# Optimization experiments

Hardware: AMD Instinct MI355X
Metric: run time of the kernel (lower is better)

## Reference

```python
import jax, jax.numpy as jnp
import numpy as np
from jax import lax

B, T = 256, 512
D_DEC, D_ENC2, D_ATT = 512, 1024, 128
N_FILT, K = 32, 31
PAD = (K - 1) // 2


def setup_inputs() -> dict:
    key = jax.random.key(0)
    ks = jax.random.split(key, 10)
    s = 0.02
    return {
        "query": jax.random.normal(ks[0], (B, D_DEC), jnp.float32),
        "encoder_output": jax.random.normal(ks[1], (B, T, D_ENC2), jnp.float32),
        "attention_weights": jax.random.uniform(ks[2], (B, T), jnp.float32),
        "Wq": jax.random.normal(ks[3], (D_DEC, D_ATT), jnp.float32) * s,
        "Wk": jax.random.normal(ks[4], (D_ENC2, D_ATT), jnp.float32) * s,
        "Wv": jax.random.normal(ks[5], (D_ENC2, D_DEC), jnp.float32) * s,
        "Wloc": jax.random.normal(ks[6], (N_FILT, D_ATT), jnp.float32) * s,
        "conv_w": jax.random.normal(ks[7], (N_FILT, 1, K), jnp.float32) * s,
        "conv_b": jax.random.normal(ks[8], (N_FILT,), jnp.float32) * s,
        "Wscore": jax.random.normal(ks[9], (D_ATT, 1), jnp.float32) * s,
    }


def reference(query, encoder_output, attention_weights, Wq, Wk, Wv, Wloc, conv_w, conv_b, Wscore):
    # query projection: (B, D_att), broadcast over time
    q = (query @ Wq)[:, None, :]                      # (B, 1, D_att)
    k = encoder_output @ Wk                           # (B, T, D_att)
    # location features: conv1d over previous attention weights
    loc = lax.conv_general_dilated(
        attention_weights[:, None, :],                # (B, 1, T)
        conv_w,                                       # (F, 1, K)
        window_strides=(1,),
        padding=[(PAD, PAD)],
        dimension_numbers=("NCH", "OIH", "NCH"),
    ) + conv_b[None, :, None]                         # (B, F, T)
    loc = jnp.einsum("bft,fa->bta", loc, Wloc)        # (B, T, D_att)
    energy = jnp.tanh(q + k + loc) @ Wscore           # (B, T, 1)
    new_w = jax.nn.softmax(energy[..., 0], axis=1)    # (B, T)
    context = jnp.einsum("bt,btd->bd", new_w, encoder_output) @ Wv  # (B, D_dec)
    return context, new_w
```

## Files before the change

kernel.cpp:

```cpp
#include <hip/hip_runtime.h>
#include <hip/hip_bf16.h>

typedef __attribute__((ext_vector_type(8))) short bf16x8;
typedef __attribute__((ext_vector_type(4))) float f32x4;

#define NB   256
#define TT   512
#define DDEC 512
#define DENC 1024
#define DATT 128
#define NF   32
#define KW   31
#define PW   15

struct SMem {
  union {
    struct {
      __hip_bfloat16 locA[512][40];
      __hip_bfloat16 locBt[128][40];
    } l;
    float part[16][1024];
  } u;
  float qpart[8][128];
  float attw[TT];
  float qrow[DDEC];
  float cw[NF][32];
  float cb[NF];
  float qv[DATT];
  float wsc[DATT];
  float energy[TT];
  float red[16];
  float scal[2];
};

__device__ __forceinline__ float fast_tanh(float x) {
  float e = __expf(2.f * x);
  return 1.f - 2.f / (e + 1.f);
}

__global__ __launch_bounds__(256) void prep_wkt(const float* __restrict__ Wk,
                                                __hip_bfloat16* __restrict__ WkT) {
  int idx = blockIdx.x * 256 + threadIdx.x;
  int k2 = idx >> 7, a = idx & 127;
  int k = k2 * 2;
  union { ushort2 u; __hip_bfloat16 h[2]; } cv;
  cv.h[0] = __float2bfloat16(Wk[(size_t)k * DATT + a]);
  cv.h[1] = __float2bfloat16(Wk[(size_t)(k + 1) * DATT + a]);
  *reinterpret_cast<ushort2*>(WkT + (size_t)a * 1024 + k) = cv.u;
}

__global__ __launch_bounds__(1024) void pass1_kernel(
    const float* __restrict__ query,
    const float* __restrict__ enc,
    const float* __restrict__ attw,
    const float* __restrict__ Wq,
    const __hip_bfloat16* __restrict__ WkT,
    const float* __restrict__ Wloc,
    const float* __restrict__ convw,
    const float* __restrict__ convb,
    const float* __restrict__ wscore,
    float* __restrict__ out_w,
    float* __restrict__ ctx_enc) {
  __shared__ SMem sm;
  const int b    = blockIdx.x;
  const int tid  = threadIdx.x;
  const int lane = tid & 63;
  const int wv   = tid >> 6;
  const int lrow = lane & 15;
  const int lgrp = lane >> 4;

  if (tid < TT) {
    sm.attw[tid] = attw[(size_t)b * TT + tid];
    sm.qrow[tid] = query[(size_t)b * DDEC + tid];
  }
  if (tid < NF * KW) sm.cw[tid / KW][tid % KW] = convw[tid];
  if (tid < NF)   sm.cb[tid]  = convb[tid];
  if (tid < DATT) sm.wsc[tid] = wscore[tid];
  for (int i = tid; i < NF * DATT; i += 1024) {
    int f = i >> 7, a = i & 127;
    sm.u.l.locBt[a][f] = __float2bfloat16(Wloc[i]);
  }
  __syncthreads();

  {
    const int p = tid >> 7, a = tid & 127;
    float acc = 0.f;
    const float* wq = Wq + (size_t)(p * 64) * DATT + a;
#pragma unroll 8
    for (int d = 0; d < 64; ++d)
      acc = fmaf(sm.qrow[p * 64 + d], wq[(size_t)d * DATT], acc);
    sm.qpart[p][a] = acc;
  }
  {
    const int t = tid & 511, h = tid >> 9;
#pragma unroll
    for (int f0 = 0; f0 < 16; ++f0) {
      const int f = h * 16 + f0;
      float acc = sm.cb[f];
      for (int k = 0; k < KW; ++k) {
        int ts = t - PW + k;
        float x = (ts >= 0 && ts < TT) ? sm.attw[ts] : 0.f;
        acc = fmaf(sm.cw[f][k], x, acc);
      }
      sm.u.l.locA[t][f] = __float2bfloat16(acc);
    }
  }
  __syncthreads();
  if (tid < DATT) {
    float s = 0.f;
#pragma unroll
    for (int p = 0; p < 8; ++p) s += sm.qpart[p][tid];
    sm.qv[tid] = s;
  }

  f32x4 acc[2][8];
  {
    bf16x8 af[2], bfr[8];
#pragma unroll
    for (int m = 0; m < 2; ++m)
      af[m] = *reinterpret_cast<const bf16x8*>(
          &sm.u.l.locA[wv * 32 + m * 16 + lrow][lgrp * 8]);
#pragma unroll
    for (int n = 0; n < 8; ++n)
      bfr[n] = *reinterpret_cast<const bf16x8*>(
          &sm.u.l.locBt[n * 16 + lrow][lgrp * 8]);
#pragma unroll
    for (int m = 0; m < 2; ++m)
#pragma unroll
      for (int n = 0; n < 8; ++n)
        acc[m][n] = __builtin_amdgcn_mfma_f32_16x16x32_bf16(
            af[m], bfr[n], (f32x4){0.f, 0.f, 0.f, 0.f}, 0, 0, 0);
  }
  __syncthreads();

  const float* pa0 = enc + (((size_t)b * TT) + wv * 32 + lrow) * DENC + lgrp * 8;
  const __hip_bfloat16* pb = WkT + lrow * 1024 + lgrp * 8;

  for (int c = 0; c < 16; ++c) {
    const int k0 = c * 64;
#pragma unroll
    for (int s = 0; s < 2; ++s) {
      const int ko = k0 + s * 32;
      bf16x8 af[2];
#pragma unroll
      for (int m = 0; m < 2; ++m) {
        const float* p = pa0 + (size_t)m * 16 * DENC + ko;
        float4 v0 = *reinterpret_cast<const float4*>(p);
        float4 v1 = *reinterpret_cast<const float4*>(p + 4);
        union { bf16x8 v; __hip_bfloat16 h[8]; } cv;
        cv.h[0] = __float2bfloat16(v0.x); cv.h[1] = __float2bfloat16(v0.y);
        cv.h[2] = __float2bfloat16(v0.z); cv.h[3] = __float2bfloat16(v0.w);
        cv.h[4] = __float2bfloat16(v1.x); cv.h[5] = __float2bfloat16(v1.y);
        cv.h[6] = __float2bfloat16(v1.z); cv.h[7] = __float2bfloat16(v1.w);
        af[m] = cv.v;
      }
      bf16x8 bfr[8];
#pragma unroll
      for (int n = 0; n < 8; ++n)
        bfr[n] = *reinterpret_cast<const bf16x8*>(pb + (size_t)n * 16 * 1024 + ko);
#pragma unroll
      for (int m = 0; m < 2; ++m)
#pragma unroll
        for (int n = 0; n < 8; ++n)
          acc[m][n] = __builtin_amdgcn_mfma_f32_16x16x32_bf16(
              af[m], bfr[n], acc[m][n], 0, 0, 0);
    }
  }

#pragma unroll
  for (int m = 0; m < 2; ++m) {
#pragma unroll
    for (int r = 0; r < 4; ++r) {
      float e = 0.f;
#pragma unroll
      for (int n = 0; n < 8; ++n) {
        int col = n * 16 + lrow;
        float v = acc[m][n][r] + sm.qv[col];
        e = fmaf(fast_tanh(v), sm.wsc[col], e);
      }
      e += __shfl_xor(e, 1);
      e += __shfl_xor(e, 2);
      e += __shfl_xor(e, 4);
      e += __shfl_xor(e, 8);
      if (lrow == 0) sm.energy[wv * 32 + m * 16 + lgrp * 4 + r] = e;
    }
  }
  __syncthreads();

  const float e0 = (tid < TT) ? sm.energy[tid] : -1e30f;
  float m1 = e0;
#pragma unroll
  for (int off = 1; off < 64; off <<= 1) m1 = fmaxf(m1, __shfl_xor(m1, off));
  if (lane == 0) sm.red[wv] = m1;
  __syncthreads();
  if (tid == 0) {
    float mm = sm.red[0];
#pragma unroll
    for (int i = 1; i < 16; ++i) mm = fmaxf(mm, sm.red[i]);
    sm.scal[0] = mm;
  }
  __syncthreads();
  const float ex = (tid < TT) ? __expf(e0 - sm.scal[0]) : 0.f;
  float s1 = ex;
#pragma unroll
  for (int off = 1; off < 64; off <<= 1) s1 += __shfl_xor(s1, off);
  if (lane == 0) sm.red[wv] = s1;
  __syncthreads();
  if (tid == 0) {
    float ss = 0.f;
#pragma unroll
    for (int i = 0; i < 16; ++i) ss += sm.red[i];
    sm.scal[1] = 1.f / ss;
  }
  __syncthreads();
  if (tid < TT) {
    const float wnorm = ex * sm.scal[1];
    sm.energy[tid] = wnorm;
    out_w[(size_t)b * TT + tid] = wnorm;
  }
  __syncthreads();

  float4 a0 = {0,0,0,0}, a1 = {0,0,0,0}, a2 = {0,0,0,0}, a3 = {0,0,0,0};
  const int t0 = wv * 32;
  for (int tt = 0; tt < 32; ++tt) {
    const int t = t0 + tt;
    const float wt = sm.energy[t];
    const float4* row =
        reinterpret_cast<const float4*>(enc + ((size_t)b * TT + t) * DENC);
    float4 v0 = row[lane];
    float4 v1 = row[64 + lane];
    float4 v2 = row[128 + lane];
    float4 v3 = row[192 + lane];
    a0.x = fmaf(wt, v0.x, a0.x); a0.y = fmaf(wt, v0.y, a0.y);
    a0.z = fmaf(wt, v0.z, a0.z); a0.w = fmaf(wt, v0.w, a0.w);
    a1.x = fmaf(wt, v1.x, a1.x); a1.y = fmaf(wt, v1.y, a1.y);
    a1.z = fmaf(wt, v1.z, a1.z); a1.w = fmaf(wt, v1.w, a1.w);
    a2.x = fmaf(wt, v2.x, a2.x); a2.y = fmaf(wt, v2.y, a2.y);
    a2.z = fmaf(wt, v2.z, a2.z); a2.w = fmaf(wt, v2.w, a2.w);
    a3.x = fmaf(wt, v3.x, a3.x); a3.y = fmaf(wt, v3.y, a3.y);
    a3.z = fmaf(wt, v3.z, a3.z); a3.w = fmaf(wt, v3.w, a3.w);
  }
  *reinterpret_cast<float4*>(&sm.u.part[wv][lane * 4])       = a0;
  *reinterpret_cast<float4*>(&sm.u.part[wv][256 + lane * 4]) = a1;
  *reinterpret_cast<float4*>(&sm.u.part[wv][512 + lane * 4]) = a2;
  *reinterpret_cast<float4*>(&sm.u.part[wv][768 + lane * 4]) = a3;
  __syncthreads();
  {
    const int d = tid;
    float s = 0.f;
#pragma unroll
    for (int w = 0; w < 16; ++w) s += sm.u.part[w][d];
    ctx_enc[(size_t)b * DENC + d] = s;
  }
}

__global__ __launch_bounds__(512) void ctx_proj_kernel(
    const float* __restrict__ ctx_enc,
    const float* __restrict__ Wv,
    float* __restrict__ out) {
  __shared__ float sc[DENC];
  const int b = blockIdx.x, tid = threadIdx.x;
  for (int i = tid; i < DENC; i += 512) sc[i] = ctx_enc[(size_t)b * DENC + i];
  __syncthreads();
  float acc = 0.f;
#pragma unroll 8
  for (int d = 0; d < DENC; ++d)
    acc = fmaf(sc[d], Wv[(size_t)d * DDEC + tid], acc);
  out[(size_t)b * DDEC + tid] = acc;
}

extern "C" void kernel_launch(void* const* d_in, const int* in_sizes, int n_in,
                              void* d_out, int out_size, void* d_ws, size_t ws_size,
                              hipStream_t stream) {
  const float* query  = (const float*)d_in[0];
  const float* enc    = (const float*)d_in[1];
  const float* attw   = (const float*)d_in[2];
  const float* Wq     = (const float*)d_in[3];
  const float* Wk     = (const float*)d_in[4];
  const float* Wv     = (const float*)d_in[5];
  const float* Wloc   = (const float*)d_in[6];
  const float* convw  = (const float*)d_in[7];
  const float* convb  = (const float*)d_in[8];
  const float* wscore = (const float*)d_in[9];

  float* ctx     = (float*)d_out;
  float* neww    = (float*)d_out + NB * TT;
  float* ctx_enc = (float*)d_ws;
  __hip_bfloat16* WkT =
      (__hip_bfloat16*)((char*)d_ws + (size_t)NB * DENC * sizeof(float));

  hipLaunchKernelGGL(prep_wkt, dim3(256), dim3(256), 0, stream, Wk, WkT);
  hipLaunchKernelGGL(pass1_kernel, dim3(NB), dim3(1024), 0, stream,
                     query, enc, attw, Wq, WkT, Wloc, convw, convb, wscore,
                     neww, ctx_enc);
  hipLaunchKernelGGL(ctx_proj_kernel, dim3(NB), dim3(512), 0, stream,
                     ctx_enc, Wv, ctx);
}
```

Baseline: 390.9 us.

## Double-buffer encoder tiles into LDS via async global_load_lds in K-loop

Replaces the direct per-lane float4 global loads of encoder rows in the key-projection MFMA loop with asynchronous global-to-LDS copies, using a per-wave double buffer and an XOR swizzle. The next 32-column chunk is prefetched while the current one is converted to bf16 and fed to the MFMAs, with explicit vmcnt waits and scheduling barriers. The aim is to hide global memory latency on the dominant encoder stream. It adds 128KB of LDS use through the union and relies on hand-counted vmcnt values, which could lower occupancy or break if the load counts change.

After: 353.7 us. 1.11x faster.

```diff
diff --git a/kernel.cpp b/kernel.cpp
--- a/kernel.cpp
+++ b/kernel.cpp
@@ -13,12 +13,18 @@
 #define KW   31
 #define PW   15
 
+#define GLDS16(g, l)                                                        \
+  __builtin_amdgcn_global_load_lds(                                         \
+      (const __attribute__((address_space(1))) void*)(uintptr_t)(g),        \
+      (__attribute__((address_space(3))) void*)(uintptr_t)(l), 16, 0, 0)
+
 struct SMem {
   union {
     struct {
       __hip_bfloat16 locA[512][40];
       __hip_bfloat16 locBt[128][40];
     } l;
+    char astage[16 * 8192];
     float part[16][1024];
   } u;
   float qpart[8][128];
@@ -133,39 +139,70 @@
   }
   __syncthreads();
 
-  const float* pa0 = enc + (((size_t)b * TT) + wv * 32 + lrow) * DENC + lgrp * 8;
-  const __hip_bfloat16* pb = WkT + lrow * 1024 + lgrp * 8;
-
-  for (int c = 0; c < 16; ++c) {
-    const int k0 = c * 64;
-#pragma unroll
-    for (int s = 0; s < 2; ++s) {
-      const int ko = k0 + s * 32;
-      bf16x8 af[2];
-#pragma unroll
-      for (int m = 0; m < 2; ++m) {
-        const float* p = pa0 + (size_t)m * 16 * DENC + ko;
-        float4 v0 = *reinterpret_cast<const float4*>(p);
-        float4 v1 = *reinterpret_cast<const float4*>(p + 4);
-        union { bf16x8 v; __hip_bfloat16 h[8]; } cv;
-        cv.h[0] = __float2bfloat16(v0.x); cv.h[1] = __float2bfloat16(v0.y);
-        cv.h[2] = __float2bfloat16(v0.z); cv.h[3] = __float2bfloat16(v0.w);
-        cv.h[4] = __float2bfloat16(v1.x); cv.h[5] = __float2bfloat16(v1.y);
-        cv.h[6] = __float2bfloat16(v1.z); cv.h[7] = __float2bfloat16(v1.w);
-        af[m] = cv.v;
-      }
-      bf16x8 bfr[8];
+  char* abase = sm.u.astage + wv * 8192;
+  const int srow  = lane >> 3;
+  const int swcol = ((lane & 7) ^ srow) * 4;
+  const float* gs = enc + ((size_t)b * TT + wv * 32 + srow) * DENC + swcol;
+
+  auto STAGE = [&](int p, int c) {
+    const float* g0 = gs + c * 32;
+    char* d0 = abase + p * 4096;
+#pragma unroll
+    for (int i = 0; i < 4; ++i)
+      GLDS16(g0 + (size_t)i * 8 * DENC, d0 + i * 1024);
+  };
+
+  bf16x8 bfr[8];
+  auto LOADB = [&](int c) {
+    const __hip_bfloat16* pbc = WkT + (size_t)lrow * 1024 + lgrp * 8 + c * 32;
+#pragma unroll
+    for (int n = 0; n < 8; ++n)
+      bfr[n] = *reinterpret_cast<const bf16x8*>(pbc + (size_t)n * 16 * 1024);
+  };
+
+  auto COMPUTE = [&](int cur) {
+    const char* rb = abase + cur * 4096;
+    bf16x8 af[2];
+#pragma unroll
+    for (int m = 0; m < 2; ++m) {
+      const int row = m * 16 + lrow;
+      const int x = (row & 7) << 4;
+      float4 f0 = *reinterpret_cast<const float4*>(
+          rb + row * 128 + ((lgrp * 32) ^ x));
+      float4 f1 = *reinterpret_cast<const float4*>(
+          rb + row * 128 + ((lgrp * 32 + 16) ^ x));
+      union { bf16x8 v; __hip_bfloat16 h[8]; } cv;
+      cv.h[0] = __float2bfloat16(f0.x); cv.h[1] = __float2bfloat16(f0.y);
+      cv.h[2] = __float2bfloat16(f0.z); cv.h[3] = __float2bfloat16(f0.w);
+      cv.h[4] = __float2bfloat16(f1.x); cv.h[5] = __float2bfloat16(f1.y);
+      cv.h[6] = __float2bfloat16(f1.z); cv.h[7] = __float2bfloat16(f1.w);
+      af[m] = cv.v;
+    }
+#pragma unroll
+    for (int m = 0; m < 2; ++m)
 #pragma unroll
       for (int n = 0; n < 8; ++n)
-        bfr[n] = *reinterpret_cast<const bf16x8*>(pb + (size_t)n * 16 * 1024 + ko);
-#pragma unroll
-      for (int m = 0; m < 2; ++m)
-#pragma unroll
-        for (int n = 0; n < 8; ++n)
-          acc[m][n] = __builtin_amdgcn_mfma_f32_16x16x32_bf16(
-              af[m], bfr[n], acc[m][n], 0, 0, 0);
-    }
-  }
+        acc[m][n] = __builtin_amdgcn_mfma_f32_16x16x32_bf16(
+            af[m], bfr[n], acc[m][n], 0, 0, 0);
+  };
+
+  STAGE(0, 0);
+  int cur = 0;
+#pragma unroll 1
+  for (int c = 0; c < 31; ++c) {
+    LOADB(c);
+    STAGE(cur ^ 1, c + 1);
+    __builtin_amdgcn_sched_barrier(0);
+    asm volatile("s_waitcnt vmcnt(12)" ::: "memory");
+    __builtin_amdgcn_sched_barrier(0);
+    COMPUTE(cur);
+    cur ^= 1;
+  }
+  LOADB(31);
+  __builtin_amdgcn_sched_barrier(0);
+  asm volatile("s_waitcnt vmcnt(8)" ::: "memory");
+  __builtin_amdgcn_sched_barrier(0);
+  COMPUTE(cur);
 
 #pragma unroll
   for (int m = 0; m < 2; ++m) {
```

## Rewrite main kernel as single-pass flash-style online softmax with LDS-staged encoder tiles

Applied to the files above, without the earlier changes.

Replaces the two-read structure (energy GEMM reading encoder rows, then a second global pass for the weighted context sum) with a tiled loop over time. Each 16-row tile is double-buffered into LDS via global_load_lds with an XOR swizzle, then reused for both the Wk projection (MFMA, split-K across waves with LDS atomic adds) and the context accumulation, using an online max/sum softmax. This is meant to halve global reads of the large encoder tensor and overlap loads with compute. In exchange it adds per-tile barriers, LDS atomics, a split-K reduction, and rescaling work, and the location features are recomputed per tile with scalar loops.

Result: slower. 1.285 ms (+228.7%).

```diff
diff --git a/kernel.cpp b/kernel.cpp
--- a/kernel.cpp
+++ b/kernel.cpp
@@ -12,30 +12,46 @@
 #define NF   32
 #define KW   31
 #define PW   15
+#define TR   16
+#define NTILE 32
+
+#define GLDS16(g, l)                                                        \
+  __builtin_amdgcn_global_load_lds(                                         \
+      (const __attribute__((address_space(1))) void*)(uintptr_t)(g),        \
+      (__attribute__((address_space(3))) void*)(uintptr_t)(l), 16, 0, 0)
 
 struct SMem {
-  union {
-    struct {
-      __hip_bfloat16 locA[512][40];
-      __hip_bfloat16 locBt[128][40];
-    } l;
-    float part[16][1024];
-  } u;
-  float qpart[8][128];
+  float buf[2][TR][1024];
+  float E[TR][137];
+  __hip_bfloat16 wlocT[DATT][36];
   float attw[TT];
   float qrow[DDEC];
-  float cw[NF][32];
+  float cw[NF][KW + 1];
   float cb[NF];
   float qv[DATT];
   float wsc[DATT];
-  float energy[TT];
-  float red[16];
-  float scal[2];
+  float locf[TR][34];
+  float e_red[TR];
+  float e_save[TT];
 };
 
 __device__ __forceinline__ float fast_tanh(float x) {
   float e = __expf(2.f * x);
   return 1.f - 2.f / (e + 1.f);
+}
+
+__device__ __forceinline__ void memfence_sched() {
+  __builtin_amdgcn_sched_barrier(0);
+  asm volatile("" ::: "memory");
+}
+__device__ __forceinline__ void bar_raw() {
+  memfence_sched();
+  __builtin_amdgcn_s_barrier();
+  memfence_sched();
+}
+__device__ __forceinline__ void bar_lgkm() {
+  asm volatile("s_waitcnt lgkmcnt(0)" ::: "memory");
+  bar_raw();
 }
 
 __global__ __launch_bounds__(256) void prep_wkt(const float* __restrict__ Wk,
@@ -49,10 +65,10 @@
   *reinterpret_cast<ushort2*>(WkT + (size_t)a * 1024 + k) = cv.u;
 }
 
-__global__ __launch_bounds__(1024) void pass1_kernel(
+__global__ __launch_bounds__(1024) void flash_kernel(
     const float* __restrict__ query,
     const float* __restrict__ enc,
-    const float* __restrict__ attw,
+    const float* __restrict__ attwg,
     const float* __restrict__ Wq,
     const __hip_bfloat16* __restrict__ WkT,
     const float* __restrict__ Wloc,
@@ -62,15 +78,13 @@
     float* __restrict__ out_w,
     float* __restrict__ ctx_enc) {
   __shared__ SMem sm;
-  const int b    = blockIdx.x;
-  const int tid  = threadIdx.x;
-  const int lane = tid & 63;
-  const int wv   = tid >> 6;
-  const int lrow = lane & 15;
-  const int lgrp = lane >> 4;
+  const int b = blockIdx.x, tid = threadIdx.x;
+  const int lane = tid & 63, wv = tid >> 6;
+  const int lrow = lane & 15, lgrp = lane >> 4;
+  const int ks = wv >> 1, ch = wv & 1;
 
   if (tid < TT) {
-    sm.attw[tid] = attw[(size_t)b * TT + tid];
+    sm.attw[tid] = attwg[(size_t)b * TT + tid];
     sm.qrow[tid] = query[(size_t)b * DDEC + tid];
   }
   if (tid < NF * KW) sm.cw[tid / KW][tid % KW] = convw[tid];
@@ -78,180 +92,162 @@
   if (tid < DATT) sm.wsc[tid] = wscore[tid];
   for (int i = tid; i < NF * DATT; i += 1024) {
     int f = i >> 7, a = i & 127;
-    sm.u.l.locBt[a][f] = __float2bfloat16(Wloc[i]);
-  }
-  __syncthreads();
+    sm.wlocT[a][f] = __float2bfloat16(Wloc[i]);
+  }
+
+  bf16x8 bfr[4][4];
+#pragma unroll
+  for (int s = 0; s < 4; ++s)
+#pragma unroll
+    for (int n = 0; n < 4; ++n)
+      bfr[s][n] = *reinterpret_cast<const bf16x8*>(
+          WkT + (size_t)(ch * 64 + n * 16 + lrow) * 1024 + ks * 128 + s * 32 + lgrp * 8);
+
+  auto STAGE = [&](int p, int t) {
+    const float* gsrc = enc + ((size_t)b * TT + t * TR + wv) * DENC;
+    char* dst = (char*)&sm.buf[p][wv][0];
+    const int swz = ((lane & 7) ^ (wv & 7)) | (lane & 56);
+#pragma unroll
+    for (int i = 0; i < 4; ++i)
+      GLDS16(gsrc + (size_t)(i * 64 + swz) * 4, dst + i * 1024);
+  };
+
+  STAGE(0, 0);
+  bar_lgkm();
 
   {
+    float* qp = &sm.E[0][0];
     const int p = tid >> 7, a = tid & 127;
     float acc = 0.f;
     const float* wq = Wq + (size_t)(p * 64) * DATT + a;
 #pragma unroll 8
-    for (int d = 0; d < 64; ++d)
-      acc = fmaf(sm.qrow[p * 64 + d], wq[(size_t)d * DATT], acc);
-    sm.qpart[p][a] = acc;
-  }
+    for (int dd = 0; dd < 64; ++dd)
+      acc = fmaf(sm.qrow[p * 64 + dd], wq[(size_t)dd * DATT], acc);
+    qp[p * 128 + a] = acc;
+  }
+  bar_lgkm();
+  if (tid < DATT) {
+    float* qp = &sm.E[0][0];
+    float s = 0.f;
+#pragma unroll
+    for (int p = 0; p < 8; ++p) s += qp[p * 128 + tid];
+    sm.qv[tid] = s;
+  }
+  bar_lgkm();
   {
-    const int t = tid & 511, h = tid >> 9;
-#pragma unroll
-    for (int f0 = 0; f0 < 16; ++f0) {
-      const int f = h * 16 + f0;
-      float acc = sm.cb[f];
-      for (int k = 0; k < KW; ++k) {
-        int ts = t - PW + k;
-        float x = (ts >= 0 && ts < TT) ? sm.attw[ts] : 0.f;
-        acc = fmaf(sm.cw[f][k], x, acc);
+    int i0 = tid * 2;
+    sm.E[i0 >> 7][i0 & 127] = 0.f;
+    sm.E[(i0 + 1) >> 7][(i0 + 1) & 127] = 0.f;
+  }
+  bar_lgkm();
+
+  float m_run = -INFINITY, l_run = 0.f, ctxv = 0.f;
+  const int d = tid;
+
+#pragma unroll 1
+  for (int t = 0; t < NTILE; ++t) {
+    const int cur = t & 1;
+    if (t + 1 < NTILE) {
+      STAGE(cur ^ 1, t + 1);
+      __builtin_amdgcn_sched_barrier(0);
+      asm volatile("s_waitcnt vmcnt(4)" ::: "memory");
+    } else {
+      asm volatile("s_waitcnt vmcnt(0)" ::: "memory");
+    }
+    bar_raw();
+
+    const char* rb = (const char*)&sm.buf[cur][0][0];
+
+    f32x4 acc[4];
+#pragma unroll
+    for (int n = 0; n < 4; ++n) acc[n] = (f32x4){0.f, 0.f, 0.f, 0.f};
+#pragma unroll
+    for (int s = 0; s < 4; ++s) {
+      const int c0 = ks * 32 + s * 8 + lgrp * 2;
+      const int sl0 = c0 ^ (lrow & 7);
+      const int sl1 = (c0 + 1) ^ (lrow & 7);
+      float4 f0 = *reinterpret_cast<const float4*>(rb + lrow * 4096 + sl0 * 16);
+      float4 f1 = *reinterpret_cast<const float4*>(rb + lrow * 4096 + sl1 * 16);
+      union { bf16x8 v; __hip_bfloat16 h[8]; } cv;
+      cv.h[0] = __float2bfloat16(f0.x); cv.h[1] = __float2bfloat16(f0.y);
+      cv.h[2] = __float2bfloat16(f0.z); cv.h[3] = __float2bfloat16(f0.w);
+      cv.h[4] = __float2bfloat16(f1.x); cv.h[5] = __float2bfloat16(f1.y);
+      cv.h[6] = __float2bfloat16(f1.z); cv.h[7] = __float2bfloat16(f1.w);
+#pragma unroll
+      for (int n = 0; n < 4; ++n)
+        acc[n] = __builtin_amdgcn_mfma_f32_16x16x32_bf16(cv.v, bfr[s][n], acc[n], 0, 0, 0);
+    }
+#pragma unroll
+    for (int n = 0; n < 4; ++n)
+#pragma unroll
+      for (int r = 0; r < 4; ++r)
+        atomicAdd(&sm.E[lgrp * 4 + r][ch * 64 + n * 16 + lrow], acc[n][r]);
+    bar_lgkm();
+
+    {
+      const int grow = t * TR + wv;
+      if (lane < NF) {
+        float a = sm.cb[lane];
+#pragma unroll
+        for (int k = 0; k < KW; ++k) {
+          int ts = grow - PW + k;
+          float x = (ts >= 0 && ts < TT) ? sm.attw[ts] : 0.f;
+          a = fmaf(sm.cw[lane][k], x, a);
+        }
+        sm.locf[wv][lane] = a;
       }
-      sm.u.l.locA[t][f] = __float2bfloat16(acc);
-    }
-  }
-  __syncthreads();
-  if (tid < DATT) {
-    float s = 0.f;
-#pragma unroll
-    for (int p = 0; p < 8; ++p) s += sm.qpart[p][tid];
-    sm.qv[tid] = s;
-  }
-
-  f32x4 acc[2][8];
-  {
-    bf16x8 af[2], bfr[8];
-#pragma unroll
-    for (int m = 0; m < 2; ++m)
-      af[m] = *reinterpret_cast<const bf16x8*>(
-          &sm.u.l.locA[wv * 32 + m * 16 + lrow][lgrp * 8]);
-#pragma unroll
-    for (int n = 0; n < 8; ++n)
-      bfr[n] = *reinterpret_cast<const bf16x8*>(
-          &sm.u.l.locBt[n * 16 + lrow][lgrp * 8]);
-#pragma unroll
-    for (int m = 0; m < 2; ++m)
-#pragma unroll
-      for (int n = 0; n < 8; ++n)
-        acc[m][n] = __builtin_amdgcn_mfma_f32_16x16x32_bf16(
-            af[m], bfr[n], (f32x4){0.f, 0.f, 0.f, 0.f}, 0, 0, 0);
-  }
-  __syncthreads();
-
-  const float* pa0 = enc + (((size_t)b * TT) + wv * 32 + lrow) * DENC + lgrp * 8;
-  const __hip_bfloat16* pb = WkT + lrow * 1024 + lgrp * 8;
-
-  for (int c = 0; c < 16; ++c) {
-    const int k0 = c * 64;
-#pragma unroll
-    for (int s = 0; s < 2; ++s) {
-      const int ko = k0 + s * 32;
-      bf16x8 af[2];
-#pragma unroll
-      for (int m = 0; m < 2; ++m) {
-        const float* p = pa0 + (size_t)m * 16 * DENC + ko;
-        float4 v0 = *reinterpret_cast<const float4*>(p);
-        float4 v1 = *reinterpret_cast<const float4*>(p + 4);
-        union { bf16x8 v; __hip_bfloat16 h[8]; } cv;
-        cv.h[0] = __float2bfloat16(v0.x); cv.h[1] = __float2bfloat16(v0.y);
-        cv.h[2] = __float2bfloat16(v0.z); cv.h[3] = __float2bfloat16(v0.w);
-        cv.h[4] = __float2bfloat16(v1.x); cv.h[5] = __float2bfloat16(v1.y);
-        cv.h[6] = __float2bfloat16(v1.z); cv.h[7] = __float2bfloat16(v1.w);
-        af[m] = cv.v;
+      asm volatile("s_waitcnt lgkmcnt(0)" ::: "memory");
+      __builtin_amdgcn_sched_barrier(0);
+      float ep = 0.f;
+#pragma unroll
+      for (int h = 0; h < 2; ++h) {
+        const int a = lane + h * 64;
+        float lf = 0.f;
+        const __hip_bfloat16* wl = &sm.wlocT[a][0];
+#pragma unroll
+        for (int f = 0; f < NF; ++f)
+          lf = fmaf(sm.locf[wv][f], __bfloat162float(wl[f]), lf);
+        float v = sm.E[wv][a] + sm.qv[a] + lf;
+        ep = fmaf(fast_tanh(v), sm.wsc[a], ep);
       }
-      bf16x8 bfr[8];
-#pragma unroll
-      for (int n = 0; n < 8; ++n)
-        bfr[n] = *reinterpret_cast<const bf16x8*>(pb + (size_t)n * 16 * 1024 + ko);
-#pragma unroll
-      for (int m = 0; m < 2; ++m)
-#pragma unroll
-        for (int n = 0; n < 8; ++n)
-          acc[m][n] = __builtin_amdgcn_mfma_f32_16x16x32_bf16(
-              af[m], bfr[n], acc[m][n], 0, 0, 0);
-    }
-  }
-
-#pragma unroll
-  for (int m = 0; m < 2; ++m) {
-#pragma unroll
-    for (int r = 0; r < 4; ++r) {
-      float e = 0.f;
-#pragma unroll
-      for (int n = 0; n < 8; ++n) {
-        int col = n * 16 + lrow;
-        float v = acc[m][n][r] + sm.qv[col];
-        e = fmaf(fast_tanh(v), sm.wsc[col], e);
+#pragma unroll
+      for (int off = 1; off < 64; off <<= 1) ep += __shfl_xor(ep, off);
+      if (lane == 0) { sm.e_red[wv] = ep; sm.e_save[grow] = ep; }
+    }
+    bar_lgkm();
+
+    {
+      float er[16];
+#pragma unroll
+      for (int r = 0; r < 16; ++r) er[r] = sm.e_red[r];
+      float mt = er[0];
+#pragma unroll
+      for (int r = 1; r < 16; ++r) mt = fmaxf(mt, er[r]);
+      float m_new = fmaxf(m_run, mt);
+      float fac = __expf(m_run - m_new);
+      ctxv *= fac;
+      float psum = 0.f;
+#pragma unroll
+      for (int r = 0; r < 16; ++r) {
+        float pr = __expf(er[r] - m_new);
+        psum += pr;
+        float ev = *reinterpret_cast<const float*>(
+            rb + r * 4096 + ((((d >> 2) ^ (r & 7)) << 4) | ((d & 3) << 2)));
+        ctxv = fmaf(pr, ev, ctxv);
       }
-      e += __shfl_xor(e, 1);
-      e += __shfl_xor(e, 2);
-      e += __shfl_xor(e, 4);
-      e += __shfl_xor(e, 8);
-      if (lrow == 0) sm.energy[wv * 32 + m * 16 + lgrp * 4 + r] = e;
-    }
-  }
-  __syncthreads();
-
-  const float e0 = (tid < TT) ? sm.energy[tid] : -1e30f;
-  float m1 = e0;
-#pragma unroll
-  for (int off = 1; off < 64; off <<= 1) m1 = fmaxf(m1, __shfl_xor(m1, off));
-  if (lane == 0) sm.red[wv] = m1;
-  __syncthreads();
-  if (tid == 0) {
-    float mm = sm.red[0];
-#pragma unroll
-    for (int i = 1; i < 16; ++i) mm = fmaxf(mm, sm.red[i]);
-    sm.scal[0] = mm;
-  }
-  __syncthreads();
-  const float ex = (tid < TT) ? __expf(e0 - sm.scal[0]) : 0.f;
-  float s1 = ex;
-#pragma unroll
-  for (int off = 1; off < 64; off <<= 1) s1 += __shfl_xor(s1, off);
-  if (lane == 0) sm.red[wv] = s1;
-  __syncthreads();
-  if (tid == 0) {
-    float ss = 0.f;
-#pragma unroll
-    for (int i = 0; i < 16; ++i) ss += sm.red[i];
-    sm.scal[1] = 1.f / ss;
-  }
-  __syncthreads();
-  if (tid < TT) {
-    const float wnorm = ex * sm.scal[1];
-    sm.energy[tid] = wnorm;
-    out_w[(size_t)b * TT + tid] = wnorm;
-  }
-  __syncthreads();
-
-  float4 a0 = {0,0,0,0}, a1 = {0,0,0,0}, a2 = {0,0,0,0}, a3 = {0,0,0,0};
-  const int t0 = wv * 32;
-  for (int tt = 0; tt < 32; ++tt) {
-    const int t = t0 + tt;
-    const float wt = sm.energy[t];
-    const float4* row =
-        reinterpret_cast<const float4*>(enc + ((size_t)b * TT + t) * DENC);
-    float4 v0 = row[lane];
-    float4 v1 = row[64 + lane];
-    float4 v2 = row[128 + lane];
-    float4 v3 = row[192 + lane];
-    a0.x = fmaf(wt, v0.x, a0.x); a0.y = fmaf(wt, v0.y, a0.y);
-    a0.z = fmaf(wt, v0.z, a0.z); a0.w = fmaf(wt, v0.w, a0.w);
-    a1.x = fmaf(wt, v1.x, a1.x); a1.y = fmaf(wt, v1.y, a1.y);
-    a1.z = fmaf(wt, v1.z, a1.z); a1.w = fmaf(wt, v1.w, a1.w);
-    a2.x = fmaf(wt, v2.x, a2.x); a2.y = fmaf(wt, v2.y, a2.y);
-    a2.z = fmaf(wt, v2.z, a2.z); a2.w = fmaf(wt, v2.w, a2.w);
-    a3.x = fmaf(wt, v3.x, a3.x); a3.y = fmaf(wt, v3.y, a3.y);
-    a3.z = fmaf(wt, v3.z, a3.z); a3.w = fmaf(wt, v3.w, a3.w);
-  }
-  *reinterpret_cast<float4*>(&sm.u.part[wv][lane * 4])       = a0;
-  *reinterpret_cast<float4*>(&sm.u.part[wv][256 + lane * 4]) = a1;
-  *reinterpret_cast<float4*>(&sm.u.part[wv][512 + lane * 4]) = a2;
-  *reinterpret_cast<float4*>(&sm.u.part[wv][768 + lane * 4]) = a3;
-  __syncthreads();
-  {
-    const int d = tid;
-    float s = 0.f;
-#pragma unroll
-    for (int w = 0; w < 16; ++w) s += sm.u.part[w][d];
-    ctx_enc[(size_t)b * DENC + d] = s;
-  }
+      l_run = l_run * fac + psum;
+      m_run = m_new;
+      int i0 = tid * 2;
+      sm.E[i0 >> 7][i0 & 127] = 0.f;
+      sm.E[(i0 + 1) >> 7][(i0 + 1) & 127] = 0.f;
+    }
+    bar_lgkm();
+  }
+
+  float invl = 1.f / l_run;
+  if (tid < TT)
+    out_w[(size_t)b * TT + tid] = __expf(sm.e_save[tid] - m_run) * invl;
+  ctx_enc[(size_t)b * DENC + d] = ctxv * invl;
 }
 
 __global__ __launch_bounds__(512) void ctx_proj_kernel(
@@ -264,8 +260,8 @@
   __syncthreads();
   float acc = 0.f;
 #pragma unroll 8
-  for (int d = 0; d < DENC; ++d)
-    acc = fmaf(sc[d], Wv[(size_t)d * DDEC + tid], acc);
+  for (int dd = 0; dd < DENC; ++dd)
+    acc = fmaf(sc[dd], Wv[(size_t)dd * DDEC + tid], acc);
   out[(size_t)b * DDEC + tid] = acc;
 }
 
@@ -290,7 +286,7 @@
       (__hip_bfloat16*)((char*)d_ws + (size_t)NB * DENC * sizeof(float));
 
   hipLaunchKernelGGL(prep_wkt, dim3(256), dim3(256), 0, stream, Wk, WkT);
-  hipLaunchKernelGGL(pass1_kernel, dim3(NB), dim3(1024), 0, stream,
+  hipLaunchKernelGGL(flash_kernel, dim3(NB), dim3(1024), 0, stream,
                      query, enc, attw, Wq, WkT, Wloc, convw, convb, wscore,
                      neww, ctx_enc);
   hipLaunchKernelGGL(ctx_proj_kernel, dim3(NB), dim3(512), 0, stream,
```
